# Kernel tuning notes

Measured on AMD Instinct MI355X. Metric: run time of the kernel, lower is better.

The kernel has to match this reference:

```python
import jax, jax.numpy as jnp
import numpy as np

EPS = 1e-5
NEG_SLOPE = 0.2


def setup_inputs() -> dict:
    key = jax.random.key(0)
    ks = jax.random.split(key, 8)
    N, E = 100000, 1600000
    x = jax.random.normal(ks[0], (N, 256), dtype=jnp.float32)
    adj_row = jnp.sort(jax.random.randint(ks[1], (E,), 0, N, dtype=jnp.int32))
    adj_col = jax.random.randint(ks[2], (E,), 0, N, dtype=jnp.int32)
    adj_vals = jax.random.uniform(ks[3], (E,), dtype=jnp.float32)
    # xavier_uniform-style scale
    def xavier(k, fan_in, fan_out):
        lim = float(np.sqrt(6.0 / (fan_in + fan_out)))
        return jax.random.uniform(k, (fan_in, fan_out), minval=-lim, maxval=lim, dtype=jnp.float32)
    W1 = xavier(ks[4], 256, 128)
    W2 = xavier(ks[5], 128, 128)
    W3 = xavier(ks[6], 128, 64)
    W4 = xavier(ks[7], 64, 32)
    return {"x": x, "adj_row": adj_row, "adj_col": adj_col, "adj_vals": adj_vals,
            "W1": W1, "W2": W2, "W3": W3, "W4": W4}


def _gnn_layer(h, row, col, vals, W, n_nodes):
    # support = h @ W ; out = spmm(adj, support) ; leaky_relu
    support = h @ W                          # [N, out]
    msg = support[col] * vals[:, None]       # [E, out] gather + scale
    agg = jax.ops.segment_sum(msg, row, num_segments=n_nodes)
    return jax.nn.leaky_relu(agg, NEG_SLOPE)


def _bn(h):
    # BatchNorm1d(affine=False, track_running_stats=False): batch stats, biased var
    mean = jnp.mean(h, axis=0)
    var = jnp.var(h, axis=0)
    return (h - mean) * jax.lax.rsqrt(var + EPS)


def reference(x, adj_row, adj_col, adj_vals, W1, W2, W3, W4):
    n = x.shape[0]
    h1 = _bn(jax.nn.elu(_gnn_layer(x, adj_row, adj_col, adj_vals, W1, n)))
    h2 = _bn(jax.nn.elu(_gnn_layer(h1, adj_row, adj_col, adj_vals, W2, n)))
    h3 = _bn(jax.nn.elu(_gnn_layer(h2, adj_row, adj_col, adj_vals, W3, n)))
    h4 = _bn(jax.nn.elu(_gnn_layer(h3, adj_row, adj_col, adj_vals, W4, n)))
    return (h1, h2, h3, h4)
```

## Files before the change

kernel.cpp:

```cpp
#include <hip/hip_runtime.h>
#include <hip/hip_bf16.h>

typedef __attribute__((ext_vector_type(8))) short short8;
typedef __attribute__((ext_vector_type(4))) float floatx4;
typedef __attribute__((ext_vector_type(8))) unsigned short ushortx8;

__device__ __forceinline__ float b2f(unsigned short u) {
    return __uint_as_float(((unsigned int)u) << 16);
}
__device__ __forceinline__ unsigned short f2b(float f) {
    __hip_bfloat16 b = __float2bfloat16(f);
    return *(unsigned short*)&b;
}
__device__ __forceinline__ float act_elu_lrelu(float x) {
    return x >= 0.f ? x : expm1f(0.2f * x);
}

__device__ __forceinline__ void gload16(const void* g, void* l) {
    __builtin_amdgcn_global_load_lds(
        (__attribute__((address_space(1))) void*)(g),
        (__attribute__((address_space(3))) void*)(l), 16, 0, 0);
}
#define SB() __builtin_amdgcn_sched_barrier(0)
#define WAITVM12()                                       \
    do {                                                 \
        asm volatile("s_waitcnt vmcnt(12)" ::: "memory"); \
        __builtin_amdgcn_sched_barrier(0);               \
    } while (0)

__global__ void build_rowptr(const int* __restrict__ row, int* __restrict__ rp,
                             int E, int N) {
    int e = blockIdx.x * blockDim.x + threadIdx.x;
    if (e >= E) return;
    int r = row[e];
    int rprev = (e == 0) ? -1 : row[e - 1];
    for (int q = rprev + 1; q <= r; ++q) rp[q] = e;
    if (e == E - 1) {
        for (int q = r + 1; q <= N; ++q) rp[q] = E;
    }
}

__global__ __launch_bounds__(256) void wprep(
    const float* __restrict__ W1, const float* __restrict__ W2,
    const float* __restrict__ W3, const float* __restrict__ W4,
    unsigned short* __restrict__ B1, unsigned short* __restrict__ B2,
    unsigned short* __restrict__ B3, unsigned short* __restrict__ B4) {
    int i = blockIdx.x * 256 + threadIdx.x;
    const float* W;
    unsigned short* Wb;
    int CIN, COUT, idx;
    if (i < 32768) {
        W = W1; Wb = B1; CIN = 256; COUT = 128; idx = i;
    } else if (i < 49152) {
        W = W2; Wb = B2; CIN = 128; COUT = 128; idx = i - 32768;
    } else if (i < 57344) {
        W = W3; Wb = B3; CIN = 128; COUT = 64; idx = i - 49152;
    } else if (i < 59392) {
        W = W4; Wb = B4; CIN = 64; COUT = 32; idx = i - 57344;
    } else {
        return;
    }
    int k = idx / COUT, n = idx % COUT;
    int kc = k >> 3, kr = k & 7;
    Wb[((size_t)n * (CIN / 8) + (kc ^ (n & 7))) * 8 + kr] =
        (unsigned short)f2b(W[idx]);
}

template <int CIN, int COUT, bool NORM>
__global__ __launch_bounds__(256) void gemm_mfma(
    float* H, const unsigned short* __restrict__ Wb,
    unsigned short* __restrict__ S, const float* __restrict__ st, float invN,
    int Nrows) {
    constexpr int CHALF = COUT / 2;
    constexpr int NCHUNK = CIN / 8;
    __shared__ short Wt[CIN * CHALF];

    int wave = threadIdx.x >> 6, lane = threadIdx.x & 63;
    int m = lane & 15, quad = lane >> 4;
    int r0 = blockIdx.x * 64 + wave * 16;
    int rowi = r0 + m;
    int rowc = rowi < Nrows ? rowi : (Nrows - 1);

    short8 a[CIN / 32];
    const float* hrow = H + (size_t)rowc * CIN;
#pragma unroll
    for (int ks = 0; ks < CIN / 32; ++ks) {
        int c0 = ks * 32 + quad * 8;
        const float* p = hrow + c0;
        floatx4 x0 = *(const floatx4*)p;
        floatx4 x1 = *(const floatx4*)(p + 4);
        if constexpr (NORM) {
            floatx4 s0 = *(const floatx4*)(st + c0);
            floatx4 s1 = *(const floatx4*)(st + c0 + 4);
            floatx4 q0 = *(const floatx4*)(st + CIN + c0);
            floatx4 q1 = *(const floatx4*)(st + CIN + c0 + 4);
#pragma unroll
            for (int j = 0; j < 4; ++j) {
                float mean = s0[j] * invN;
                float var = q0[j] * invN - mean * mean;
                x0[j] = (x0[j] - mean) * rsqrtf(fmaxf(var, 0.f) + 1e-5f);
                mean = s1[j] * invN;
                var = q1[j] * invN - mean * mean;
                x1[j] = (x1[j] - mean) * rsqrtf(fmaxf(var, 0.f) + 1e-5f);
            }
            if (rowi < Nrows) {
                float* op = H + (size_t)rowi * CIN + c0;
                __builtin_nontemporal_store(x0, (floatx4*)op);
                __builtin_nontemporal_store(x1, (floatx4*)(op + 4));
            }
        }
        short8 t;
#pragma unroll
        for (int j = 0; j < 4; ++j) {
            t[j] = (short)f2b(x0[j]);
            t[4 + j] = (short)f2b(x1[j]);
        }
        a[ks] = t;
    }

#pragma unroll
    for (int h = 0; h < 2; ++h) {
        {
            constexpr int CHUNKS = CIN * CHALF / 8;
            const short8* src = (const short8*)(Wb + h * CIN * CHALF);
            short8* dst = (short8*)Wt;
            for (int i = threadIdx.x; i < CHUNKS; i += 256) dst[i] = src[i];
        }
        __syncthreads();

#pragma unroll
        for (int nt = 0; nt < CHALF / 16; ++nt) {
            floatx4 acc = {0.f, 0.f, 0.f, 0.f};
            int nn = nt * 16 + m;
#pragma unroll
            for (int ks = 0; ks < CIN / 32; ++ks) {
                int kc = ks * 4 + quad;
                short8 b =
                    *(const short8*)(&Wt[(nn * NCHUNK + (kc ^ (nn & 7))) * 8]);
                acc = __builtin_amdgcn_mfma_f32_16x16x32_bf16(a[ks], b, acc, 0,
                                                              0, 0);
            }
            int n = h * CHALF + nn;
#pragma unroll
            for (int reg = 0; reg < 4; ++reg) {
                int rr = r0 + quad * 4 + reg;
                if (rr < Nrows) S[(size_t)rr * COUT + n] = f2b(acc[reg]);
            }
        }
        __syncthreads();
    }
}

template <int C>
__global__ __launch_bounds__(256) void spmm_act_stats(
    const ushortx8* __restrict__ S8, const int* __restrict__ colIdx,
    const float* __restrict__ vals, const int* __restrict__ rowPtr,
    float* __restrict__ Ag, float* __restrict__ stats, int N) {
    constexpr int LPN = C / 8;
    constexpr int NPB = 256 / LPN;
    __shared__ char stage[4 * 2 * 4096];

    int tid = threadIdx.x;
    int sub = tid / LPN;
    int lc = tid % LPN;
    int wave = tid >> 6;
    int lane = tid & 63;
    char* wbase = stage + wave * 8192;

    float s[8], s2[8];
#pragma unroll
    for (int j = 0; j < 8; ++j) { s[j] = 0.f; s2[j] = 0.f; }

    int ngroups = (N + NPB - 1) / NPB;
    for (int g = blockIdx.x; g < ngroups; g += gridDim.x) {
        int node = g * NPB + sub;
        int nc = node < N ? node : N - 1;
        int e0 = rowPtr[nc];
        int e1 = node < N ? rowPtr[nc + 1] : e0;
        int len = e1 - e0;
        int wl = len;
#pragma unroll
        for (int mm = LPN; mm < 64; mm <<= 1) {
            int o = __shfl_xor(wl, mm, 64);
            wl = o > wl ? o : wl;
        }
        int tmax = (wl + 3) >> 2;
        if (tmax == 0) continue;

        auto ce = [&](int i) {
            int q = i < e1 - 1 ? i : e1 - 1;
            return q > 0 ? q : 0;
        };

        float acc[8];
#pragma unroll
        for (int j = 0; j < 8; ++j) acc[j] = 0.f;

        int c0t[4];
#pragma unroll
        for (int k = 0; k < 4; ++k) c0t[k] = colIdx[ce(e0 + k)];
        SB();
        int ca[4];
#pragma unroll
        for (int k = 0; k < 4; ++k) ca[k] = colIdx[ce(e0 + 4 + k)];
        SB();
#pragma unroll
        for (int k = 0; k < 4; ++k)
            gload16(&S8[(size_t)c0t[k] * LPN + lc], wbase + k * 1024);
        SB();
        float vc[4];
#pragma unroll
        for (int k = 0; k < 4; ++k) vc[k] = vals[ce(e0 + k)];
        SB();

        for (int t = 0; t < tmax; ++t) {
            int slot = t & 1;
            int cb[4];
            int b2 = e0 + t * 4 + 8;
#pragma unroll
            for (int k = 0; k < 4; ++k) cb[k] = colIdx[ce(b2 + k)];
            SB();
            WAITVM12();
            char* dst = wbase + (slot ^ 1) * 4096;
#pragma unroll
            for (int k = 0; k < 4; ++k)
                gload16(&S8[(size_t)ca[k] * LPN + lc], dst + k * 1024);
            SB();
            float vn[4];
            int b1 = e0 + t * 4 + 4;
#pragma unroll
            for (int k = 0; k < 4; ++k) vn[k] = vals[ce(b1 + k)];
            SB();
            WAITVM12();
            const char* src = wbase + slot * 4096 + lane * 16;
            int b0 = e0 + t * 4;
#pragma unroll
            for (int k = 0; k < 4; ++k) {
                ushortx8 gk = *(const ushortx8*)(src + k * 1024);
                float v = (b0 + k < e1) ? vc[k] : 0.f;
#pragma unroll
                for (int j = 0; j < 8; ++j) acc[j] += v * b2f(gk[j]);
            }
#pragma unroll
            for (int k = 0; k < 4; ++k) { ca[k] = cb[k]; vc[k] = vn[k]; }
        }

        if (node < N) {
            floatx4 r0, r1;
#pragma unroll
            for (int j = 0; j < 4; ++j) {
                float a0 = act_elu_lrelu(acc[j]);
                float a1 = act_elu_lrelu(acc[4 + j]);
                r0[j] = a0;
                r1[j] = a1;
                s[j] += a0;
                s2[j] += a0 * a0;
                s[4 + j] += a1;
                s2[4 + j] += a1 * a1;
            }
            float* op = Ag + (size_t)node * C + lc * 8;
            *(floatx4*)op = r0;
            *(floatx4*)(op + 4) = r1;
        }
    }

    __syncthreads();
    float* sh = (float*)stage;
#pragma unroll
    for (int j = 0; j < 8; ++j) {
        sh[(0 * NPB + sub) * C + lc * 8 + j] = s[j];
        sh[(1 * NPB + sub) * C + lc * 8 + j] = s2[j];
    }
    __syncthreads();
    if (tid < C) {
        float t0 = 0.f, t1 = 0.f;
        for (int gg = 0; gg < NPB; ++gg) {
            t0 += sh[(0 * NPB + gg) * C + tid];
            t1 += sh[(1 * NPB + gg) * C + tid];
        }
        atomicAdd(&stats[tid], t0);
        atomicAdd(&stats[C + tid], t1);
    }
}

template <int C>
__global__ __launch_bounds__(256) void bn_norm(
    float* __restrict__ Ag, const float* __restrict__ stats, int N) {
    constexpr int RPB = 256 / C;
    int c = threadIdx.x % C;
    int rg = threadIdx.x / C;
    float invN = 1.f / (float)N;
    float mean = stats[c] * invN;
    float var = stats[C + c] * invN - mean * mean;
    float inv = rsqrtf(fmaxf(var, 0.f) + 1e-5f);
    for (int r = blockIdx.x * RPB + rg; r < N; r += gridDim.x * RPB) {
        float x = Ag[(size_t)r * C + c];
        Ag[(size_t)r * C + c] = (x - mean) * inv;
    }
}

extern "C" void kernel_launch(void* const* d_in, const int* in_sizes, int n_in,
                              void* d_out, int out_size, void* d_ws,
                              size_t ws_size, hipStream_t stream) {
    const float* x = (const float*)d_in[0];
    const int* adj_row = (const int*)d_in[1];
    const int* adj_col = (const int*)d_in[2];
    const float* adj_vals = (const float*)d_in[3];
    const float* W1 = (const float*)d_in[4];
    const float* W2 = (const float*)d_in[5];
    const float* W3 = (const float*)d_in[6];
    const float* W4 = (const float*)d_in[7];

    int N = in_sizes[0] / 256;
    int E = in_sizes[1];

    char* ws = (char*)d_ws;
    int* rp = (int*)ws;
    size_t off = (((size_t)(N + 1) * 4) + 255) & ~(size_t)255;
    float* stats = (float*)(ws + off);
    off += 4 * 256 * sizeof(float);
    unsigned short* Wb1 = (unsigned short*)(ws + off); off += 32768 * 2;
    unsigned short* Wb2 = (unsigned short*)(ws + off); off += 16384 * 2;
    unsigned short* Wb3 = (unsigned short*)(ws + off); off += 8192 * 2;
    unsigned short* Wb4 = (unsigned short*)(ws + off); off += 2048 * 2;
    off = (off + 255) & ~(size_t)255;
    unsigned short* S = (unsigned short*)(ws + off);

    hipMemsetAsync(stats, 0, 4 * 256 * sizeof(float), stream);
    build_rowptr<<<(E + 255) / 256, 256, 0, stream>>>(adj_row, rp, E, N);
    wprep<<<232, 256, 0, stream>>>(W1, W2, W3, W4, Wb1, Wb2, Wb3, Wb4);

    float* h1 = (float*)d_out;
    float* h2 = h1 + (size_t)N * 128;
    float* h3 = h2 + (size_t)N * 128;
    float* h4 = h3 + (size_t)N * 64;

    float invN = 1.f / (float)N;
    int gblk = (N + 63) / 64;
    auto sgrid = [](int N, int npb) {
        int ng = (N + npb - 1) / npb;
        return ng < 2048 ? ng : 2048;
    };

    gemm_mfma<256, 128, false><<<gblk, 256, 0, stream>>>(
        (float*)x, Wb1, S, nullptr, invN, N);
    spmm_act_stats<128><<<sgrid(N, 16), 256, 0, stream>>>(
        (const ushortx8*)S, adj_col, adj_vals, rp, h1, stats + 0, N);

    gemm_mfma<128, 128, true><<<gblk, 256, 0, stream>>>(
        h1, Wb2, S, stats + 0, invN, N);
    spmm_act_stats<128><<<sgrid(N, 16), 256, 0, stream>>>(
        (const ushortx8*)S, adj_col, adj_vals, rp, h2, stats + 256, N);

    gemm_mfma<128, 64, true><<<gblk, 256, 0, stream>>>(
        h2, Wb3, S, stats + 256, invN, N);
    spmm_act_stats<64><<<sgrid(N, 32), 256, 0, stream>>>(
        (const ushortx8*)S, adj_col, adj_vals, rp, h3, stats + 512, N);

    gemm_mfma<64, 32, true><<<gblk, 256, 0, stream>>>(
        h3, Wb4, S, stats + 512, invN, N);
    spmm_act_stats<32><<<sgrid(N, 64), 256, 0, stream>>>(
        (const ushortx8*)S, adj_col, adj_vals, rp, h4, stats + 768, N);
    bn_norm<32><<<256, 256, 0, stream>>>(h4, stats + 768, N);
}
```

Before: 607.5 us.

## Sort nodes by degree and pack padded col/val pairs for balanced SpMM

Adds a preprocessing pipeline (degree histogram, scan, scatter into a permutation, per-16-node group max length, packed float2 col/val arrays padded to the group length) so each SpMM wave handles nodes of similar degree. The SpMM loop then reads interleaved col/val pairs with no clamping or masking, and outputs are scattered through the permutation. This targets load imbalance and divergence from varying row lengths, and cuts the separate index and value loads. In exchange it adds several setup kernels, extra workspace, and atomics. It also swaps expm1f for __expf minus one in the activation.

```diff
diff --git a/kernel.cpp b/kernel.cpp
--- a/kernel.cpp
+++ b/kernel.cpp
@@ -13,7 +13,7 @@
     return *(unsigned short*)&b;
 }
 __device__ __forceinline__ float act_elu_lrelu(float x) {
-    return x >= 0.f ? x : expm1f(0.2f * x);
+    return x >= 0.f ? x : (__expf(0.2f * x) - 1.f);
 }
 
 __device__ __forceinline__ void gload16(const void* g, void* l) {
@@ -22,10 +22,10 @@
         (__attribute__((address_space(3))) void*)(l), 16, 0, 0);
 }
 #define SB() __builtin_amdgcn_sched_barrier(0)
-#define WAITVM12()                                       \
-    do {                                                 \
-        asm volatile("s_waitcnt vmcnt(12)" ::: "memory"); \
-        __builtin_amdgcn_sched_barrier(0);               \
+#define WAITVM(n)                                               \
+    do {                                                        \
+        asm volatile("s_waitcnt vmcnt(" #n ")" ::: "memory");   \
+        __builtin_amdgcn_sched_barrier(0);                      \
     } while (0)
 
 __global__ void build_rowptr(const int* __restrict__ row, int* __restrict__ rp,
@@ -37,6 +37,92 @@
     for (int q = rprev + 1; q <= r; ++q) rp[q] = e;
     if (e == E - 1) {
         for (int q = r + 1; q <= N; ++q) rp[q] = E;
+    }
+}
+
+__global__ __launch_bounds__(256) void deg_hist(const int* __restrict__ rp,
+                                                int* __restrict__ hist, int N) {
+    int n = blockIdx.x * 256 + threadIdx.x;
+    if (n >= N) return;
+    int d = rp[n + 1] - rp[n];
+    atomicAdd(&hist[d < 255 ? d : 255], 1);
+}
+
+__global__ __launch_bounds__(256) void scan256(const int* __restrict__ hist,
+                                               int* __restrict__ binCur) {
+    __shared__ int tmp[256];
+    int t = threadIdx.x;
+    int v = hist[t];
+    tmp[t] = v;
+    __syncthreads();
+    for (int o = 1; o < 256; o <<= 1) {
+        int u = (t >= o) ? tmp[t - o] : 0;
+        __syncthreads();
+        tmp[t] += u;
+        __syncthreads();
+    }
+    binCur[t] = tmp[t] - v;
+}
+
+__global__ __launch_bounds__(256) void deg_scatter(const int* __restrict__ rp,
+                                                   int* __restrict__ binCur,
+                                                   int* __restrict__ perm,
+                                                   int N) {
+    int n = blockIdx.x * 256 + threadIdx.x;
+    if (n >= N) return;
+    int d = rp[n + 1] - rp[n];
+    int pos = atomicAdd(&binCur[d < 255 ? d : 255], 1);
+    perm[pos] = n;
+}
+
+__global__ __launch_bounds__(256) void grp_len(
+    const int* __restrict__ rp, const int* __restrict__ perm,
+    int* __restrict__ gL, int* __restrict__ gBase, int* __restrict__ cnt,
+    int N, int ngroups) {
+    int gi = blockIdx.x * 256 + threadIdx.x;
+    if (gi >= ngroups) return;
+    int m = 0;
+    for (int j = 0; j < 16; ++j) {
+        int p = gi * 16 + j;
+        if (p < N) {
+            int n = perm[p];
+            int d = rp[n + 1] - rp[n];
+            m = m > d ? m : d;
+        }
+    }
+    int L = (m + 3) & ~3;
+    gL[gi] = L;
+    gBase[gi] = L ? atomicAdd(cnt, 16 * L) : 0;
+}
+
+__global__ __launch_bounds__(256) void fill_packed(
+    const int* __restrict__ rp, const int* __restrict__ colIdx,
+    const float* __restrict__ vals, const int* __restrict__ perm,
+    const int* __restrict__ gL, const int* __restrict__ gBase,
+    float2* __restrict__ packed, int N, int Npos) {
+    int w = (blockIdx.x * 256 + threadIdx.x) >> 6;
+    int lane = threadIdx.x & 63;
+    if (w >= Npos) return;
+    int gi = w >> 4;
+    int L = gL[gi];
+    if (L == 0) return;
+    float2* dst = packed + (size_t)gBase[gi] + (size_t)(w & 15) * L;
+    int d = 0, e0 = 0;
+    if (w < N) {
+        int n = perm[w];
+        e0 = rp[n];
+        d = rp[n + 1] - e0;
+    }
+    for (int j = lane; j < L; j += 64) {
+        float2 v;
+        if (j < d) {
+            v.x = __int_as_float(colIdx[e0 + j]);
+            v.y = vals[e0 + j];
+        } else {
+            v.x = __int_as_float(0);
+            v.y = 0.f;
+        }
+        dst[j] = v;
     }
 }
 
@@ -153,99 +239,97 @@
 
 template <int C>
 __global__ __launch_bounds__(256) void spmm_act_stats(
-    const ushortx8* __restrict__ S8, const int* __restrict__ colIdx,
-    const float* __restrict__ vals, const int* __restrict__ rowPtr,
-    float* __restrict__ Ag, float* __restrict__ stats, int N) {
+    const char* __restrict__ Sb, const float2* __restrict__ packed,
+    const int* __restrict__ gBase, const int* __restrict__ gL,
+    const int* __restrict__ perm, float* __restrict__ Ag,
+    float* __restrict__ stats, int N, int Npos) {
     constexpr int LPN = C / 8;
     constexpr int NPB = 256 / LPN;
-    __shared__ char stage[4 * 2 * 4096];
+    constexpr int SH = (C == 128) ? 8 : (C == 64) ? 7 : 6;
+    __shared__ __align__(16) char stage[4 * 2 * 4096];
 
     int tid = threadIdx.x;
-    int sub = tid / LPN;
-    int lc = tid % LPN;
-    int wave = tid >> 6;
-    int lane = tid & 63;
+    int wave = tid >> 6, lane = tid & 63;
+    int sub = tid / LPN, lc = tid % LPN;
     char* wbase = stage + wave * 8192;
+    int lcoff = lc * 16;
 
     float s[8], s2[8];
 #pragma unroll
     for (int j = 0; j < 8; ++j) { s[j] = 0.f; s2[j] = 0.f; }
 
-    int ngroups = (N + NPB - 1) / NPB;
-    for (int g = blockIdx.x; g < ngroups; g += gridDim.x) {
-        int node = g * NPB + sub;
-        int nc = node < N ? node : N - 1;
-        int e0 = rowPtr[nc];
-        int e1 = node < N ? rowPtr[nc + 1] : e0;
-        int len = e1 - e0;
-        int wl = len;
-#pragma unroll
-        for (int mm = LPN; mm < 64; mm <<= 1) {
-            int o = __shfl_xor(wl, mm, 64);
-            wl = o > wl ? o : wl;
-        }
-        int tmax = (wl + 3) >> 2;
-        if (tmax == 0) continue;
-
-        auto ce = [&](int i) {
-            int q = i < e1 - 1 ? i : e1 - 1;
-            return q > 0 ? q : 0;
-        };
-
+    int nblk = (Npos + NPB - 1) / NPB;
+    for (int blk = blockIdx.x; blk < nblk; blk += gridDim.x) {
+        int p = blk * NPB + sub;
+        int inb = p < Npos;
+        int gi = inb ? (p >> 4) : 0;
+        int L = inb ? gL[gi] : 0;
         float acc[8];
 #pragma unroll
         for (int j = 0; j < 8; ++j) acc[j] = 0.f;
 
-        int c0t[4];
-#pragma unroll
-        for (int k = 0; k < 4; ++k) c0t[k] = colIdx[ce(e0 + k)];
-        SB();
-        int ca[4];
-#pragma unroll
-        for (int k = 0; k < 4; ++k) ca[k] = colIdx[ce(e0 + 4 + k)];
-        SB();
-#pragma unroll
-        for (int k = 0; k < 4; ++k)
-            gload16(&S8[(size_t)c0t[k] * LPN + lc], wbase + k * 1024);
-        SB();
-        float vc[4];
-#pragma unroll
-        for (int k = 0; k < 4; ++k) vc[k] = vals[ce(e0 + k)];
-        SB();
-
-        for (int t = 0; t < tmax; ++t) {
-            int slot = t & 1;
-            int cb[4];
-            int b2 = e0 + t * 4 + 8;
-#pragma unroll
-            for (int k = 0; k < 4; ++k) cb[k] = colIdx[ce(b2 + k)];
+        if (L) {
+            const float2* pe =
+                packed + (size_t)gBase[gi] + (size_t)(p & 15) * L;
+            int tmax = L >> 2;
+
+            float2 pkA[4], pkB[4];
+#pragma unroll
+            for (int k = 0; k < 4; ++k) pkA[k] = pe[k];
+#pragma unroll
+            for (int k = 0; k < 4; ++k) pkB[k] = pe[4 + k];
             SB();
-            WAITVM12();
-            char* dst = wbase + (slot ^ 1) * 4096;
 #pragma unroll
             for (int k = 0; k < 4; ++k)
-                gload16(&S8[(size_t)ca[k] * LPN + lc], dst + k * 1024);
+                gload16(Sb + (((unsigned)__float_as_uint(pkA[k].x) << SH) +
+                              lcoff),
+                        wbase + k * 1024);
             SB();
-            float vn[4];
-            int b1 = e0 + t * 4 + 4;
-#pragma unroll
-            for (int k = 0; k < 4; ++k) vn[k] = vals[ce(b1 + k)];
-            SB();
-            WAITVM12();
-            const char* src = wbase + slot * 4096 + lane * 16;
-            int b0 = e0 + t * 4;
-#pragma unroll
-            for (int k = 0; k < 4; ++k) {
-                ushortx8 gk = *(const ushortx8*)(src + k * 1024);
-                float v = (b0 + k < e1) ? vc[k] : 0.f;
-#pragma unroll
-                for (int j = 0; j < 8; ++j) acc[j] += v * b2f(gk[j]);
-            }
-#pragma unroll
-            for (int k = 0; k < 4; ++k) { ca[k] = cb[k]; vc[k] = vn[k]; }
-        }
-
-        if (node < N) {
+
+            for (int t = 0; t < tmax - 1; ++t) {
+                int slot = t & 1;
+                float2 pkC[4];
+                const float2* pe2 = pe + t * 4 + 8;
+#pragma unroll
+                for (int k = 0; k < 4; ++k) pkC[k] = pe2[k];
+                SB();
+                WAITVM(8);
+                char* dst = wbase + (slot ^ 1) * 4096;
+#pragma unroll
+                for (int k = 0; k < 4; ++k)
+                    gload16(Sb + (((unsigned)__float_as_uint(pkB[k].x) << SH) +
+                                  lcoff),
+                            dst + k * 1024);
+                SB();
+                WAITVM(8);
+                const char* src = wbase + slot * 4096 + lane * 16;
+#pragma unroll
+                for (int k = 0; k < 4; ++k) {
+                    ushortx8 gk = *(const ushortx8*)(src + k * 1024);
+                    float v = pkA[k].y;
+#pragma unroll
+                    for (int j = 0; j < 8; ++j) acc[j] += v * b2f(gk[j]);
+                }
+#pragma unroll
+                for (int k = 0; k < 4; ++k) { pkA[k] = pkB[k]; pkB[k] = pkC[k]; }
+            }
+
+            WAITVM(0);
+            {
+                int slot = (tmax - 1) & 1;
+                const char* src = wbase + slot * 4096 + lane * 16;
+#pragma unroll
+                for (int k = 0; k < 4; ++k) {
+                    ushortx8 gk = *(const ushortx8*)(src + k * 1024);
+                    float v = pkA[k].y;
+#pragma unroll
+                    for (int j = 0; j < 8; ++j) acc[j] += v * b2f(gk[j]);
+                }
+            }
+        }
+
+        if (p < N) {
+            int node = perm[p];
             floatx4 r0, r1;
 #pragma unroll
             for (int j = 0; j < 4; ++j) {
@@ -313,22 +397,42 @@
 
     int N = in_sizes[0] / 256;
     int E = in_sizes[1];
+    int ngroups = (N + 15) / 16;
+    int Npos = ngroups * 16;
 
     char* ws = (char*)d_ws;
-    int* rp = (int*)ws;
-    size_t off = (((size_t)(N + 1) * 4) + 255) & ~(size_t)255;
-    float* stats = (float*)(ws + off);
-    off += 4 * 256 * sizeof(float);
-    unsigned short* Wb1 = (unsigned short*)(ws + off); off += 32768 * 2;
-    unsigned short* Wb2 = (unsigned short*)(ws + off); off += 16384 * 2;
-    unsigned short* Wb3 = (unsigned short*)(ws + off); off += 8192 * 2;
-    unsigned short* Wb4 = (unsigned short*)(ws + off); off += 2048 * 2;
-    off = (off + 255) & ~(size_t)255;
-    unsigned short* S = (unsigned short*)(ws + off);
-
-    hipMemsetAsync(stats, 0, 4 * 256 * sizeof(float), stream);
+    size_t off = 0;
+    auto carve = [&](size_t bytes) {
+        char* p = ws + off;
+        off = (off + bytes + 255) & ~(size_t)255;
+        return p;
+    };
+    int* rp = (int*)carve((size_t)(N + 1) * 4);
+    float* stats = (float*)carve((1024 + 256 + 64) * 4);
+    int* hist = (int*)((char*)stats + 1024 * 4);
+    int* cnt = hist + 256;
+    int* binCur = (int*)carve(256 * 4);
+    unsigned short* Wb1 = (unsigned short*)carve(32768 * 2);
+    unsigned short* Wb2 = (unsigned short*)carve(16384 * 2);
+    unsigned short* Wb3 = (unsigned short*)carve(8192 * 2);
+    unsigned short* Wb4 = (unsigned short*)carve(2048 * 2);
+    int* perm = (int*)carve((size_t)Npos * 4);
+    int* gL = (int*)carve((size_t)ngroups * 4);
+    int* gBase = (int*)carve((size_t)ngroups * 4);
+    float2* packed = (float2*)carve(((size_t)E + 4 * (size_t)N + 2048) * 8);
+    unsigned short* S = (unsigned short*)carve((size_t)N * 128 * 2);
+
+    hipMemsetAsync(stats, 0, (1024 + 256 + 64) * 4, stream);
     build_rowptr<<<(E + 255) / 256, 256, 0, stream>>>(adj_row, rp, E, N);
     wprep<<<232, 256, 0, stream>>>(W1, W2, W3, W4, Wb1, Wb2, Wb3, Wb4);
+    int nb = (N + 255) / 256;
+    deg_hist<<<nb, 256, 0, stream>>>(rp, hist, N);
+    scan256<<<1, 256, 0, stream>>>(hist, binCur);
+    deg_scatter<<<nb, 256, 0, stream>>>(rp, binCur, perm, N);
+    grp_len<<<(ngroups + 255) / 256, 256, 0, stream>>>(rp, perm, gL, gBase,
+                                                       cnt, N, ngroups);
+    fill_packed<<<(Npos + 3) / 4, 256, 0, stream>>>(
+        rp, adj_col, adj_vals, perm, gL, gBase, packed, N, Npos);
 
     float* h1 = (float*)d_out;
     float* h2 = h1 + (size_t)N * 128;
@@ -337,29 +441,29 @@
 
     float invN = 1.f / (float)N;
     int gblk = (N + 63) / 64;
-    auto sgrid = [](int N, int npb) {
-        int ng = (N + npb - 1) / npb;
+    auto sgrid = [&](int npb) {
+        int ng = (Npos + npb - 1) / npb;
         return ng < 2048 ? ng : 2048;
     };
 
     gemm_mfma<256, 128, false><<<gblk, 256, 0, stream>>>(
         (float*)x, Wb1, S, nullptr, invN, N);
-    spmm_act_stats<128><<<sgrid(N, 16), 256, 0, stream>>>(
-        (const ushortx8*)S, adj_col, adj_vals, rp, h1, stats + 0, N);
+    spmm_act_stats<128><<<sgrid(16), 256, 0, stream>>>(
+        (const char*)S, packed, gBase, gL, perm, h1, stats + 0, N, Npos);
 
     gemm_mfma<128, 128, true><<<gblk, 256, 0, stream>>>(
         h1, Wb2, S, stats + 0, invN, N);
-    spmm_act_stats<128><<<sgrid(N, 16), 256, 0, stream>>>(
-        (const ushortx8*)S, adj_col, adj_vals, rp, h2, stats + 256, N);
+    spmm_act_stats<128><<<sgrid(16), 256, 0, stream>>>(
+        (const char*)S, packed, gBase, gL, perm, h2, stats + 256, N, Npos);
 
     gemm_mfma<128, 64, true><<<gblk, 256, 0, stream>>>(
         h2, Wb3, S, stats + 256, invN, N);
-    spmm_act_stats<64><<<sgrid(N, 32), 256, 0, stream>>>(
-        (const ushortx8*)S, adj_col, adj_vals, rp, h3, stats + 512, N);
+    spmm_act_stats<64><<<sgrid(32), 256, 0, stream>>>(
+        (const char*)S, packed, gBase, gL, perm, h3, stats + 512, N, Npos);
 
     gemm_mfma<64, 32, true><<<gblk, 256, 0, stream>>>(
         h3, Wb4, S, stats + 512, invN, N);
-    spmm_act_stats<32><<<sgrid(N, 64), 256, 0, stream>>>(
-        (const ushortx8*)S, adj_col, adj_vals, rp, h4, stats + 768, N);
+    spmm_act_stats<32><<<sgrid(64), 256, 0, stream>>>(
+        (const char*)S, packed, gBase, gL, perm, h4, stats + 768, N, Npos);
     bn_norm<32><<<256, 256, 0, stream>>>(h4, stats + 768, N);
 }
```

New measurement: 1.170 ms. +92.7%, slower.
